# Kernel optimization log

Hardware: AMD Instinct MI355X
Metric: run time of the kernel (lower is better)

The kernel has to match this reference:

```python
import jax, jax.numpy as jnp
import numpy as np

GROUPS = 32
EPS = 1e-5


def setup_inputs() -> dict:
    key = jax.random.key(0)
    ks = jax.random.split(key, 4)
    B, C, H, W = 16, 512, 32, 32
    x = jax.random.normal(ks[0], (B, C, H, W), dtype=jnp.float32)
    gamma = jnp.ones((C,), jnp.float32)
    beta = jnp.zeros((C,), jnp.float32)
    # 1x1 convs as channel GEMMs; fan-in scaled init
    w_qkv = jax.random.normal(ks[1], (3 * C, C), dtype=jnp.float32) / np.sqrt(C)
    b_qkv = jnp.zeros((3 * C,), jnp.float32)
    w_proj = jax.random.normal(ks[2], (C, C), dtype=jnp.float32) / np.sqrt(C)
    b_proj = jnp.zeros((C,), jnp.float32)
    return {"x": x, "gamma": gamma, "beta": beta, "w_qkv": w_qkv,
            "b_qkv": b_qkv, "w_proj": w_proj, "b_proj": b_proj}


def _group_norm(x, gamma, beta):
    B, C, H, W = x.shape
    xg = x.reshape(B, GROUPS, C // GROUPS, H, W)
    mu = xg.mean(axis=(2, 3, 4), keepdims=True)
    var = xg.var(axis=(2, 3, 4), keepdims=True)
    xn = ((xg - mu) * jax.lax.rsqrt(var + EPS)).reshape(B, C, H, W)
    return xn * gamma[None, :, None, None] + beta[None, :, None, None]


def reference(x, gamma, beta, w_qkv, b_qkv, w_proj, b_proj):
    B, C, H, W = x.shape
    xn = _group_norm(x, gamma, beta)
    # 1x1 conv qkv: [B, 3C, H, W]
    qkv = jnp.einsum('oc,bchw->bohw', w_qkv, xn) + b_qkv[None, :, None, None]
    qkv = qkv.reshape(B, 3, C, H * W)
    q, k, v = qkv[:, 0], qkv[:, 1], qkv[:, 2]  # each [B, C, HW]
    scale = C ** (-0.5)
    # attn[b, i, j] = softmax_j( q[b,:,i] . k[b,:,j] * scale )
    attn = jax.nn.softmax(jnp.einsum('bci,bcj->bij', q, k) * scale, axis=-1)
    # out[b, c, i] = sum_j v[b,c,j] * attn[b,i,j]
    out = jnp.einsum('bcj,bij->bci', v, attn).reshape(B, C, H, W)
    proj = jnp.einsum('oc,bchw->bohw', w_proj, out) + b_proj[None, :, None, None]
    return x + proj
```

## Files before the change

### kernel.cpp

```cpp
#include <hip/hip_runtime.h>


typedef _Float16 f16;
typedef _Float16 f16x8 __attribute__((ext_vector_type(8)));
typedef _Float16 f16x4 __attribute__((ext_vector_type(4)));
typedef float fx4 __attribute__((ext_vector_type(4)));

__device__ __forceinline__ void gload16(const f16* g, f16* l) {
    __builtin_amdgcn_global_load_lds((const __attribute__((address_space(1))) void*)g,
                                     (__attribute__((address_space(3))) void*)l, 16, 0, 0);
}

__global__ __launch_bounds__(256)
void wconv_kernel(const float* __restrict__ w, f16* __restrict__ o, int n4)
{
    int i = blockIdx.x * 256 + threadIdx.x;
    if (i < n4) {
        float4 v = *(const float4*)(w + i * 4);
        f16x4 h;
        h[0] = (f16)v.x; h[1] = (f16)v.y; h[2] = (f16)v.z; h[3] = (f16)v.w;
        *(f16x4*)(o + i * 4) = h;
    }
}

__global__ __launch_bounds__(256)
void groupnorm_kernel(const float* __restrict__ x, const float* __restrict__ gamma,
                      const float* __restrict__ beta, f16* __restrict__ xnT)
{
    __shared__ float red[256], red2[256];
    __shared__ float mu_s, rs_s;
    __shared__ __align__(16) f16 T[16][1040];
    const int blk = blockIdx.x;
    const int b = blk >> 5, g = blk & 31;
    const long base = (long)blk * 16384;
    const int tid = threadIdx.x;
    const float4* xv = (const float4*)(x + base);

    float4 xr[16];
    float s = 0.f, s2 = 0.f;
#pragma unroll
    for (int i = 0; i < 16; i++) {
        float4 v = xv[tid + i * 256];
        xr[i] = v;
        s  += v.x + v.y + v.z + v.w;
        s2 += v.x * v.x + v.y * v.y + v.z * v.z + v.w * v.w;
    }
    red[tid] = s; red2[tid] = s2;
    __syncthreads();
    for (int off = 128; off > 0; off >>= 1) {
        if (tid < off) { red[tid] += red[tid + off]; red2[tid] += red2[tid + off]; }
        __syncthreads();
    }
    if (tid == 0) {
        float mu = red[0] * (1.f / 16384.f);
        float var = red2[0] * (1.f / 16384.f) - mu * mu;
        mu_s = mu;
        rs_s = rsqrtf(var + 1e-5f);
    }
    __syncthreads();
    const float mu = mu_s, rs = rs_s;

#pragma unroll
    for (int i = 0; i < 16; i++) {
        float gm = gamma[g * 16 + i] * rs;
        float bt = beta[g * 16 + i] - mu * gm;
        float4 v = xr[i];
        f16x4 o;
        o[0] = (f16)(v.x * gm + bt);
        o[1] = (f16)(v.y * gm + bt);
        o[2] = (f16)(v.z * gm + bt);
        o[3] = (f16)(v.w * gm + bt);
        *(f16x4*)&T[i][tid * 4] = o;
    }
    __syncthreads();
#pragma unroll
    for (int i = 0; i < 8; i++) {
        int idx = tid + i * 256;
        int hw = idx >> 1;
        int half8 = (idx & 1) * 8;
        f16x8 o;
#pragma unroll
        for (int j = 0; j < 8; j++) o[j] = T[half8 + j][hw];
        long dst = ((long)b * 1024 + hw) * 512 + g * 16 + half8;
        *(f16x8*)(xnT + dst) = o;
    }
}

__global__ __launch_bounds__(256)
void softmax_kernel(f16* __restrict__ S)
{
    const int wid = blockIdx.x * 4 + (threadIdx.x >> 6);
    const int lane = threadIdx.x & 63;
    f16* p = S + (long)wid * 1024 + lane * 16;
    f16x8 h0 = *(const f16x8*)p;
    f16x8 h1 = *(const f16x8*)(p + 8);
    float v[16];
#pragma unroll
    for (int i = 0; i < 8; i++) { v[i] = (float)h0[i]; v[8 + i] = (float)h1[i]; }
    float mx = v[0];
#pragma unroll
    for (int i = 1; i < 16; i++) mx = fmaxf(mx, v[i]);
    for (int off = 32; off > 0; off >>= 1) mx = fmaxf(mx, __shfl_xor(mx, off, 64));
    float sum = 0.f;
#pragma unroll
    for (int i = 0; i < 16; i++) { v[i] = __expf(v[i] - mx); sum += v[i]; }
    for (int off = 32; off > 0; off >>= 1) sum += __shfl_xor(sum, off, 64);
    const float inv = 1.f / sum;
#pragma unroll
    for (int i = 0; i < 8; i++) { h0[i] = (f16)(v[i] * inv); h1[i] = (f16)(v[8 + i] * inv); }
    *(f16x8*)p = h0;
    *(f16x8*)(p + 8) = h1;
}

template<int MODE>
__global__ __launch_bounds__(512, 2)
void pgemm_kernel(const f16* __restrict__ Ap, const f16* __restrict__ Bp,
                  void* __restrict__ Cp, f16* __restrict__ C2p,
                  const float* __restrict__ bias, const float* __restrict__ resid,
                  float alpha, int K, int lda, int ldb, int N,
                  int nm, int tpb, int nT,
                  long sAb, long sBb, long sCb)
{
    __shared__ __align__(16) f16 As[4][256 * 32];
    __shared__ __align__(16) f16 Bs[4][128 * 32];

    const int blk = (blockIdx.x & 7) * 32 + (blockIdx.x >> 3);

    const int tid = threadIdx.x;
    const int wave = tid >> 6, lane = tid & 63;
    const int quad = lane >> 4, l15 = lane & 15;
    const int wm = (wave >> 1) * 64, wn = (wave & 1) * 64;
    const int chunkoff = (quad ^ ((l15 >> 1) & 3)) * 8;

    const int rl = lane >> 2;
    const int swzc = ((lane & 3) ^ ((rl >> 1) & 3)) * 8;
    const int RA = wave * 32;
    const int RB = wave * 16;
    const int H = K >> 5;

    for (int id = blk; id < nT; id += 256) {
        const int b  = id / tpb, r = id % tpb;
        const int m0 = (r % nm) * 256, n0 = (r / nm) * 128;
        const f16* agA = Ap + (long)b * sAb + (long)(m0 + RA + rl) * lda + swzc;
        const f16* agB = Bp + (long)b * sBb + (long)(n0 + RB + rl) * ldb + swzc;

        gload16(agA,                 &As[0][RA * 32]);
        gload16(agA + 16 * lda,      &As[0][(RA + 16) * 32]);
        gload16(agB,                 &Bs[0][RB * 32]);
        gload16(agA + 32,            &As[1][RA * 32]);
        gload16(agA + 16 * lda + 32, &As[1][(RA + 16) * 32]);
        gload16(agB + 32,            &Bs[1][RB * 32]);
        asm volatile("s_waitcnt vmcnt(3)" ::: "memory");
        __builtin_amdgcn_s_barrier();

        fx4 acc[4][4] = {};
        for (int s = 0; s < H; ++s) {
            const f16* Ab = &As[s & 3][0];
            const f16* Bb = &Bs[s & 3][0];
            const bool pre = (s + 2 < H);
            f16x8 af[4], bf[4];
#pragma unroll
            for (int fm = 0; fm < 4; fm++)
                af[fm] = *(const f16x8*)&Ab[(wm + fm * 16 + l15) * 32 + chunkoff];
#pragma unroll
            for (int fn = 0; fn < 2; fn++)
                bf[fn] = *(const f16x8*)&Bb[(wn + fn * 16 + l15) * 32 + chunkoff];
            if (pre) {
                f16* d = &As[(s + 2) & 3][0];
                gload16(agA + (long)(s + 2) * 32,            d + RA * 32);
                gload16(agA + 16 * lda + (long)(s + 2) * 32, d + (RA + 16) * 32);
            }
            __builtin_amdgcn_s_barrier();
            __builtin_amdgcn_s_setprio(1);
#pragma unroll
            for (int fm = 0; fm < 4; fm++)
#pragma unroll
                for (int fn = 0; fn < 2; fn++)
                    acc[fm][fn] = __builtin_amdgcn_mfma_f32_16x16x32_f16(af[fm], bf[fn], acc[fm][fn], 0, 0, 0);
            __builtin_amdgcn_s_setprio(0);
            __builtin_amdgcn_s_barrier();
#pragma unroll
            for (int fn = 2; fn < 4; fn++)
                bf[fn] = *(const f16x8*)&Bb[(wn + fn * 16 + l15) * 32 + chunkoff];
            if (pre)
                gload16(agB + (long)(s + 2) * 32, &Bs[(s + 2) & 3][RB * 32]);
            __builtin_amdgcn_s_setprio(1);
#pragma unroll
            for (int fm = 0; fm < 4; fm++)
#pragma unroll
                for (int fn = 2; fn < 4; fn++)
                    acc[fm][fn] = __builtin_amdgcn_mfma_f32_16x16x32_f16(af[fm], bf[fn], acc[fm][fn], 0, 0, 0);
            __builtin_amdgcn_s_setprio(0);
            if (pre)               { asm volatile("s_waitcnt vmcnt(3)" ::: "memory"); }
            else if (s == H - 2)   { asm volatile("s_waitcnt vmcnt(0)" ::: "memory"); }
            __builtin_amdgcn_s_barrier();
        }

        if (MODE == 1 && n0 >= 1024) {
#pragma unroll
            for (int tm = 0; tm < 4; tm++)
#pragma unroll
            for (int tn = 0; tn < 4; tn++) {
                int gc = n0 + wn + tn * 16 + l15;
                int gr0 = m0 + wm + tm * 16 + quad * 4;
                float bs = bias[gc];
                f16x4 o;
#pragma unroll
                for (int rr = 0; rr < 4; rr++) o[rr] = (f16)(acc[tm][tn][rr] + bs);
                *(f16x4*)(C2p + (long)b * 524288 + (long)(gc - 1024) * 1024 + gr0) = o;
            }
        } else {
#pragma unroll
            for (int tm = 0; tm < 4; tm++)
#pragma unroll
            for (int tn = 0; tn < 4; tn++) {
                int gc = n0 + wn + tn * 16 + l15;
#pragma unroll
                for (int rr = 0; rr < 4; rr++) {
                    int gr = m0 + wm + tm * 16 + quad * 4 + rr;
                    float v = acc[tm][tn][rr];
                    if (MODE == 0) {
                        v *= alpha;
                        ((f16*)Cp)[(long)b * sCb + (long)gr * N + gc] = (f16)v;
                    } else if (MODE == 1) {
                        v += bias[gc];
                        ((f16*)Cp)[(long)b * 1048576 + (long)gr * 1024 + gc] = (f16)v;
                    } else {
                        v += bias[gr];
                        long idx = (long)b * sCb + (long)gr * N + gc;
                        v += resid[idx];
                        ((float*)Cp)[idx] = v;
                    }
                }
            }
        }
    }
}

extern "C" void kernel_launch(void* const* d_in, const int* in_sizes, int n_in,
                              void* d_out, int out_size, void* d_ws, size_t ws_size,
                              hipStream_t stream)
{
    const float* x      = (const float*)d_in[0];
    const float* gamma  = (const float*)d_in[1];
    const float* beta   = (const float*)d_in[2];
    const float* w_qkv  = (const float*)d_in[3];
    const float* b_qkv  = (const float*)d_in[4];
    const float* w_proj = (const float*)d_in[5];
    const float* b_proj = (const float*)d_in[6];
    float* out = (float*)d_out;

    char* ws = (char*)d_ws;
    f16* xnT   = (f16*)(ws);
    f16* qkT   = (f16*)(ws + (16L << 20));
    f16* vbuf  = (f16*)(ws + (48L << 20));
    f16* S     = (f16*)(ws + (64L << 20));
    f16* aoutT = (f16*)(ws + (96L << 20));
    f16* wqkvh = S;
    f16* wprjh = xnT;

    wconv_kernel<<<768, 256, 0, stream>>>(w_qkv, wqkvh, 196608);

    groupnorm_kernel<<<512, 256, 0, stream>>>(x, gamma, beta, xnT);

    pgemm_kernel<1><<<256, 512, 0, stream>>>(
        xnT, wqkvh, qkT, vbuf, b_qkv, nullptr, 1.0f,
        512, 512, 512, 1536,
        4, 48, 768,
        524288L, 0L, 0L);

    wconv_kernel<<<256, 256, 0, stream>>>(w_proj, wprjh, 65536);

    pgemm_kernel<0><<<256, 512, 0, stream>>>(
        qkT, qkT + 512, S, nullptr, nullptr, nullptr, 0.04419417382415922f,
        512, 1024, 1024, 1024,
        4, 32, 512,
        1048576L, 1048576L, 1048576L);

    softmax_kernel<<<4096, 256, 0, stream>>>(S);

    pgemm_kernel<0><<<256, 512, 0, stream>>>(
        S, vbuf, aoutT, nullptr, nullptr, nullptr, 1.0f,
        1024, 1024, 1024, 512,
        4, 16, 256,
        1048576L, 524288L, 524288L);

    pgemm_kernel<2><<<256, 512, 0, stream>>>(
        wprjh, aoutT, out, nullptr, b_proj, x, 1.0f,
        512, 512, 512, 1024,
        2, 16, 256,
        0L, 524288L, 524288L);
}
```

Baseline: 230.0 us.

## Enlarge GEMM tiles to 256x256 with double-buffered LDS pipeline

The shared GEMM kernel now uses 256x256 output tiles, with each wave computing 128x64, in place of 256x128. Its four-deep split-phase prefetch pipeline is replaced by a simpler double buffer with one __syncthreads per k-step. The larger tiles are meant to raise arithmetic intensity and reduce global and LDS traffic per FLOP. In exchange they use more accumulator registers and cut the tile count, so two of the GEMMs launch only 128 blocks, leaving part of the GPU idle. The simpler sync scheme also gives up the finer load/compute interleaving of the old pipeline.

```diff
diff --git a/kernel.cpp b/kernel.cpp
--- a/kernel.cpp
+++ b/kernel.cpp
@@ -118,87 +118,71 @@
                   void* __restrict__ Cp, f16* __restrict__ C2p,
                   const float* __restrict__ bias, const float* __restrict__ resid,
                   float alpha, int K, int lda, int ldb, int N,
-                  int nm, int tpb, int nT,
+                  int nn, int tpb, int nT,
                   long sAb, long sBb, long sCb)
 {
-    __shared__ __align__(16) f16 As[4][256 * 32];
-    __shared__ __align__(16) f16 Bs[4][128 * 32];
-
-    const int blk = (blockIdx.x & 7) * 32 + (blockIdx.x >> 3);
+    __shared__ __align__(16) f16 As[2][256 * 32];
+    __shared__ __align__(16) f16 Bs[2][256 * 32];
+
+    const int G = gridDim.x;
+    const int blk = (blockIdx.x & 7) * (G >> 3) + (blockIdx.x >> 3);
 
     const int tid = threadIdx.x;
     const int wave = tid >> 6, lane = tid & 63;
     const int quad = lane >> 4, l15 = lane & 15;
-    const int wm = (wave >> 1) * 64, wn = (wave & 1) * 64;
+    const int wm = (wave >> 2) * 128, wn = (wave & 3) * 64;
     const int chunkoff = (quad ^ ((l15 >> 1) & 3)) * 8;
 
     const int rl = lane >> 2;
     const int swzc = ((lane & 3) ^ ((rl >> 1) & 3)) * 8;
     const int RA = wave * 32;
-    const int RB = wave * 16;
-    const int H = K >> 5;
-
-    for (int id = blk; id < nT; id += 256) {
+    const int nkt = K >> 5;
+
+    for (int id = blk; id < nT; id += G) {
         const int b  = id / tpb, r = id % tpb;
-        const int m0 = (r % nm) * 256, n0 = (r / nm) * 128;
+        const int m0 = (r / nn) * 256, n0 = (r % nn) * 256;
         const f16* agA = Ap + (long)b * sAb + (long)(m0 + RA + rl) * lda + swzc;
-        const f16* agB = Bp + (long)b * sBb + (long)(n0 + RB + rl) * ldb + swzc;
-
-        gload16(agA,                 &As[0][RA * 32]);
-        gload16(agA + 16 * lda,      &As[0][(RA + 16) * 32]);
-        gload16(agB,                 &Bs[0][RB * 32]);
-        gload16(agA + 32,            &As[1][RA * 32]);
-        gload16(agA + 16 * lda + 32, &As[1][(RA + 16) * 32]);
-        gload16(agB + 32,            &Bs[1][RB * 32]);
-        asm volatile("s_waitcnt vmcnt(3)" ::: "memory");
-        __builtin_amdgcn_s_barrier();
-
-        fx4 acc[4][4] = {};
-        for (int s = 0; s < H; ++s) {
-            const f16* Ab = &As[s & 3][0];
-            const f16* Bb = &Bs[s & 3][0];
-            const bool pre = (s + 2 < H);
-            f16x8 af[4], bf[4];
-#pragma unroll
-            for (int fm = 0; fm < 4; fm++)
-                af[fm] = *(const f16x8*)&Ab[(wm + fm * 16 + l15) * 32 + chunkoff];
-#pragma unroll
-            for (int fn = 0; fn < 2; fn++)
+        const f16* agB = Bp + (long)b * sBb + (long)(n0 + RA + rl) * ldb + swzc;
+
+#define STAGE(buf, t)                                                     \
+        { gload16(agA + (t) * 32,            &As[buf][RA * 32]);          \
+          gload16(agA + (t) * 32 + 16 * lda, &As[buf][(RA + 16) * 32]);   \
+          gload16(agB + (t) * 32,            &Bs[buf][RA * 32]);          \
+          gload16(agB + (t) * 32 + 16 * ldb, &Bs[buf][(RA + 16) * 32]); }
+
+        STAGE(0, 0)
+        __syncthreads();
+
+        fx4 acc[8][4] = {};
+        for (int kt = 0; kt < nkt; ++kt) {
+            const int db = kt & 1;
+            if (kt + 1 < nkt) STAGE(db ^ 1, kt + 1)
+            const f16* Ab = &As[db][0];
+            const f16* Bb = &Bs[db][0];
+            f16x8 bf[4];
+#pragma unroll
+            for (int fn = 0; fn < 4; fn++)
                 bf[fn] = *(const f16x8*)&Bb[(wn + fn * 16 + l15) * 32 + chunkoff];
-            if (pre) {
-                f16* d = &As[(s + 2) & 3][0];
-                gload16(agA + (long)(s + 2) * 32,            d + RA * 32);
-                gload16(agA + 16 * lda + (long)(s + 2) * 32, d + (RA + 16) * 32);
+#pragma unroll
+            for (int fmp = 0; fmp < 4; fmp++) {
+                f16x8 a0 = *(const f16x8*)&Ab[(wm + (fmp * 2 + 0) * 16 + l15) * 32 + chunkoff];
+                f16x8 a1 = *(const f16x8*)&Ab[(wm + (fmp * 2 + 1) * 16 + l15) * 32 + chunkoff];
+                __builtin_amdgcn_s_setprio(1);
+#pragma unroll
+                for (int fn = 0; fn < 4; fn++)
+                    acc[fmp * 2 + 0][fn] = __builtin_amdgcn_mfma_f32_16x16x32_f16(a0, bf[fn], acc[fmp * 2 + 0][fn], 0, 0, 0);
+#pragma unroll
+                for (int fn = 0; fn < 4; fn++)
+                    acc[fmp * 2 + 1][fn] = __builtin_amdgcn_mfma_f32_16x16x32_f16(a1, bf[fn], acc[fmp * 2 + 1][fn], 0, 0, 0);
+                __builtin_amdgcn_s_setprio(0);
             }
-            __builtin_amdgcn_s_barrier();
-            __builtin_amdgcn_s_setprio(1);
-#pragma unroll
-            for (int fm = 0; fm < 4; fm++)
-#pragma unroll
-                for (int fn = 0; fn < 2; fn++)
-                    acc[fm][fn] = __builtin_amdgcn_mfma_f32_16x16x32_f16(af[fm], bf[fn], acc[fm][fn], 0, 0, 0);
-            __builtin_amdgcn_s_setprio(0);
-            __builtin_amdgcn_s_barrier();
-#pragma unroll
-            for (int fn = 2; fn < 4; fn++)
-                bf[fn] = *(const f16x8*)&Bb[(wn + fn * 16 + l15) * 32 + chunkoff];
-            if (pre)
-                gload16(agB + (long)(s + 2) * 32, &Bs[(s + 2) & 3][RB * 32]);
-            __builtin_amdgcn_s_setprio(1);
-#pragma unroll
-            for (int fm = 0; fm < 4; fm++)
-#pragma unroll
-                for (int fn = 2; fn < 4; fn++)
-                    acc[fm][fn] = __builtin_amdgcn_mfma_f32_16x16x32_f16(af[fm], bf[fn], acc[fm][fn], 0, 0, 0);
-            __builtin_amdgcn_s_setprio(0);
-            if (pre)               { asm volatile("s_waitcnt vmcnt(3)" ::: "memory"); }
-            else if (s == H - 2)   { asm volatile("s_waitcnt vmcnt(0)" ::: "memory"); }
-            __builtin_amdgcn_s_barrier();
+            __syncthreads();
         }
+#undef STAGE
 
         if (MODE == 1 && n0 >= 1024) {
 #pragma unroll
-            for (int tm = 0; tm < 4; tm++)
+            for (int tm = 0; tm < 8; tm++)
 #pragma unroll
             for (int tn = 0; tn < 4; tn++) {
                 int gc = n0 + wn + tn * 16 + l15;
@@ -211,7 +195,7 @@
             }
         } else {
 #pragma unroll
-            for (int tm = 0; tm < 4; tm++)
+            for (int tm = 0; tm < 8; tm++)
 #pragma unroll
             for (int tn = 0; tn < 4; tn++) {
                 int gc = n0 + wn + tn * 16 + l15;
@@ -266,7 +250,7 @@
     pgemm_kernel<1><<<256, 512, 0, stream>>>(
         xnT, wqkvh, qkT, vbuf, b_qkv, nullptr, 1.0f,
         512, 512, 512, 1536,
-        4, 48, 768,
+        6, 24, 384,
         524288L, 0L, 0L);
 
     wconv_kernel<<<256, 256, 0, stream>>>(w_proj, wprjh, 65536);
@@ -274,20 +258,20 @@
     pgemm_kernel<0><<<256, 512, 0, stream>>>(
         qkT, qkT + 512, S, nullptr, nullptr, nullptr, 0.04419417382415922f,
         512, 1024, 1024, 1024,
-        4, 32, 512,
+        4, 16, 256,
         1048576L, 1048576L, 1048576L);
 
     softmax_kernel<<<4096, 256, 0, stream>>>(S);
 
-    pgemm_kernel<0><<<256, 512, 0, stream>>>(
+    pgemm_kernel<0><<<128, 512, 0, stream>>>(
         S, vbuf, aoutT, nullptr, nullptr, nullptr, 1.0f,
         1024, 1024, 1024, 512,
-        4, 16, 256,
+        2, 8, 128,
         1048576L, 524288L, 524288L);
 
-    pgemm_kernel<2><<<256, 512, 0, stream>>>(
+    pgemm_kernel<2><<<128, 512, 0, stream>>>(
         wprjh, aoutT, out, nullptr, b_proj, x, 1.0f,
         512, 512, 512, 1024,
-        2, 16, 256,
+        4, 8, 128,
         0L, 524288L, 524288L);
 }
```

After: 267.8 us. 1.16x slower.
